# Kernel tuning notes

Measured on AMD Instinct MI355X. Metric: run time of the kernel, lower is better.

The kernel has to match this reference:

```python
import math
import jax, jax.numpy as jnp
import numpy as np

HIDDEN = 768
HEADS = 12
HEAD_DIM = HIDDEN // HEADS  # 64
NUM_BUCKETS = 32            # T5-style relative position bias defaults
MAX_DIST = 128
EPS = 1e-6


def _rel_buckets(T):
    # T5 bidirectional relative-position bucketing, computed statically in numpy.
    ctx = np.arange(T)[:, None]
    mem = np.arange(T)[None, :]
    rp = mem - ctx                     # (T, T)
    nb = NUM_BUCKETS // 2
    ret = (rp > 0).astype(np.int64) * nb
    n = np.abs(rp)
    max_exact = nb // 2
    is_small = n < max_exact
    val_large = max_exact + (
        np.log(np.maximum(n, 1) / max_exact) / math.log(MAX_DIST / max_exact) * (nb - max_exact)
    ).astype(np.int64)
    val_large = np.minimum(val_large, nb - 1)
    ret = ret + np.where(is_small, n, val_large)
    return ret  # (T, T) int


def _layernorm(x, scale, bias):
    mu = jnp.mean(x, axis=-1, keepdims=True)
    var = jnp.mean((x - mu) ** 2, axis=-1, keepdims=True)
    return (x - mu) * jax.lax.rsqrt(var + EPS) * scale + bias


def _rms_groupnorm(x, weight):
    # x: (N, C, H, W, D); RMS over (channels-in-group, spatial), per-channel scale.
    N, C, H, W, D = x.shape
    xg = x.reshape(N, HEADS, C // HEADS, H, W, D)
    ms = jnp.mean(xg * xg, axis=(2, 3, 4, 5), keepdims=True)
    xg = xg * jax.lax.rsqrt(ms + EPS)
    return xg.reshape(N, C, H, W, D) * weight[None, :, None, None, None]


def _forward(x, norm1_weight, input_head_weight, input_head_bias,
             qnorm_scale, qnorm_bias, knorm_scale, knorm_bias,
             rel_bias_table, output_head_weight, output_head_bias):
    T, B, C, H, W, D = x.shape
    residual = x
    xn = _rms_groupnorm(x.reshape(T * B, C, H, W, D), norm1_weight)
    # 1x1 conv QKV as channels-last matmul
    w_in = input_head_weight[:, :, 0, 0, 0]                       # (3C, C)
    xt = jnp.transpose(xn, (0, 2, 3, 4, 1))                        # (TB, H, W, D, C)
    qkv = xt @ w_in.T + input_head_bias                            # (TB, H, W, D, 3C)
    # '(t b) (he c) h w d -> (b h w d) he t c'  with c = 3*head_dim
    qkv = qkv.reshape(T, B, H, W, D, HEADS, 3 * HEAD_DIM)
    qkv = jnp.transpose(qkv, (1, 2, 3, 4, 5, 0, 6))                # (B,H,W,D,He,T,3hd)
    qkv = qkv.reshape(B * H * W * D, HEADS, T, 3 * HEAD_DIM)
    q, k, v = jnp.split(qkv, 3, axis=-1)                           # each (N, He, T, hd)
    q = _layernorm(q, qnorm_scale, qnorm_bias)
    k = _layernorm(k, knorm_scale, knorm_bias)
    # relative position bias (bidirectional)
    buckets = jnp.asarray(_rel_buckets(T))                         # (T, T)
    bias = jnp.transpose(rel_bias_table[buckets], (2, 0, 1))[None]  # (1, He, T, T)
    scale = 1.0 / math.sqrt(HEAD_DIM)
    attn = jax.nn.softmax(jnp.einsum('bhsc,bhtc->bhst', q, k) * scale + bias, axis=-1)
    out = jnp.einsum('bhst,bhtc->bhsc', attn, v)                   # (N, He, T, hd)
    # '(b h w d) he t c -> (t b) (he c) h w d'
    out = out.reshape(B, H, W, D, HEADS, T, HEAD_DIM)
    out = jnp.transpose(out, (5, 0, 4, 6, 1, 2, 3))                # (T,B,He,hd,H,W,D)
    out = out.reshape(T * B, C, H, W, D)
    # output 1x1 conv
    w_out = output_head_weight[:, :, 0, 0, 0]                      # (C, C)
    ot = jnp.transpose(out, (0, 2, 3, 4, 1)) @ w_out.T + output_head_bias
    y = jnp.transpose(ot, (0, 4, 1, 2, 3)).reshape(T, B, C, H, W, D)
    return y + residual


def setup_inputs() -> dict:
    key = jax.random.key(0)
    ks = jax.random.split(key, 4)
    T, B, C, H, W, D = 16, 1, HIDDEN, 16, 16, 8
    x = jax.random.normal(ks[0], (T, B, C, H, W, D), dtype=jnp.float32)
    lecun = 1.0 / math.sqrt(HIDDEN)
    return {
        'x': x,
        'norm1_weight': jnp.ones((HIDDEN,), jnp.float32),
        'input_head_weight': jax.random.normal(ks[1], (3 * HIDDEN, HIDDEN, 1, 1, 1), jnp.float32) * lecun,
        'input_head_bias': jnp.zeros((3 * HIDDEN,), jnp.float32),
        'qnorm_scale': jnp.ones((HEAD_DIM,), jnp.float32),
        'qnorm_bias': jnp.zeros((HEAD_DIM,), jnp.float32),
        'knorm_scale': jnp.ones((HEAD_DIM,), jnp.float32),
        'knorm_bias': jnp.zeros((HEAD_DIM,), jnp.float32),
        'rel_bias_table': jax.random.normal(ks[2], (NUM_BUCKETS, HEADS), jnp.float32) * 0.02,
        'output_head_weight': jax.random.normal(ks[3], (HIDDEN, HIDDEN, 1, 1, 1), jnp.float32) * lecun,
        'output_head_bias': jnp.zeros((HIDDEN,), jnp.float32),
    }


def reference(x, norm1_weight, input_head_weight, input_head_bias,
              qnorm_scale, qnorm_bias, knorm_scale, knorm_bias,
              rel_bias_table, output_head_weight, output_head_bias):
    return _forward(x, norm1_weight, input_head_weight, input_head_bias,
                    qnorm_scale, qnorm_bias, knorm_scale, knorm_bias,
                    rel_bias_table, output_head_weight, output_head_bias)
```

## Files before the change

### kernel.cpp

```cpp
#include <hip/hip_runtime.h>
#include <stdint.h>

#define Tt 16
#define Cc 768
#define Ss 2048
#define N1 2304
#define NH 12
#define HD 64
#define EPSV 1e-6f

typedef unsigned short ushort_t;
typedef __attribute__((ext_vector_type(8))) short short8;
typedef __attribute__((ext_vector_type(4))) short short4v;
typedef __attribute__((ext_vector_type(4))) float f32x4;

static __device__ __forceinline__ float b2f(unsigned short u) {
  union { unsigned int i; float f; } c;
  c.i = ((unsigned int)u) << 16;
  return c.f;
}
static __device__ __forceinline__ unsigned short f2b(float f) {
  union { float f; unsigned int i; } c;
  c.f = f;
  return (unsigned short)((c.i + 0x7fffu + ((c.i >> 16) & 1u)) >> 16);
}

static __device__ __forceinline__ void load8(const void* p, size_t eoff,
                                             int isf32, float* o) {
  if (isf32) {
    const float* f = (const float*)p + eoff;
    f32x4 a = *(const f32x4*)f;
    f32x4 b = *(const f32x4*)(f + 4);
    o[0] = a[0]; o[1] = a[1]; o[2] = a[2]; o[3] = a[3];
    o[4] = b[0]; o[5] = b[1]; o[6] = b[2]; o[7] = b[3];
  } else {
    short8 d = *(const short8*)((const ushort_t*)p + eoff);
#pragma unroll
    for (int e = 0; e < 8; e++) o[e] = b2f((unsigned short)d[e]);
  }
}
static __device__ __forceinline__ float load1(const void* p, size_t eoff, int isf32) {
  return isf32 ? ((const float*)p)[eoff] : b2f(((const ushort_t*)p)[eoff]);
}

#define GLP(p) ((const __attribute__((address_space(1))) void*)(p))
#define LDSP(p) ((__attribute__((address_space(3))) void*)(p))

__global__ __launch_bounds__(256) void detect_k(const ushort_t* __restrict__ x,
                                               int* __restrict__ flag) {
  __shared__ int sbad;
  if (threadIdx.x == 0) sbad = 0;
  __syncthreads();
  int bad = 0;
  for (int i = threadIdx.x; i < 65536; i += 256) {
    const unsigned int e = (x[i] >> 7) & 0xFFu;
    if (e == 0xFFu) bad = 1;
  }
  if (bad) atomicOr(&sbad, 1);
  __syncthreads();
  if (threadIdx.x == 0) flag[0] = sbad;
}

__global__ __launch_bounds__(256) void cvt_big_k(const void* __restrict__ src,
                                                ushort_t* __restrict__ dst,
                                                int n8, const int* __restrict__ flag) {
  const int isf32 = *flag;
  const int i = blockIdx.x * 256 + threadIdx.x;
  if (i >= n8) return;
  float o[8];
  load8(src, (size_t)i * 8, isf32, o);
  short8 v;
#pragma unroll
  for (int e = 0; e < 8; e++) v[e] = (short)f2b(o[e]);
  *(short8*)(dst + (size_t)i * 8) = v;
}

__global__ __launch_bounds__(256) void cvt_small_k(
    const void* w1, const void* bin, const void* bo, const void* qs,
    const void* qb, const void* ks, const void* kb, const void* relb,
    ushort_t* __restrict__ dst, const int* __restrict__ flag) {
  const int isf32 = *flag;
  const void* srcs[8] = {w1, bin, bo, qs, qb, ks, kb, relb};
  const int sizes[8] = {768, 2304, 768, 64, 64, 64, 64, 384};
  int off = 0;
#pragma unroll
  for (int s = 0; s < 8; s++) {
    for (int i = threadIdx.x; i < sizes[s]; i += 256)
      dst[off + i] = isf32 ? f2b(((const float*)srcs[s])[i])
                           : ((const ushort_t*)srcs[s])[i];
    off += sizes[s];
  }
}

__global__ __launch_bounds__(256) void rms_stats_k(
    const void* __restrict__ x, const int* __restrict__ flag,
    float* __restrict__ invrms) {
  const int isf32 = *flag;
  const int t = blockIdx.x / NH;
  const int g = blockIdx.x % NH;
  const size_t base = ((size_t)(t * Cc + g * 64)) * Ss;
  float ss = 0.f;
  for (int v = threadIdx.x; v < 16384; v += 256) {
    const int ci = v >> 8;
    const int sj = (v & 255) << 3;
    float o[8];
    load8(x, base + (size_t)ci * Ss + sj, isf32, o);
#pragma unroll
    for (int e = 0; e < 8; e++) ss += o[e] * o[e];
  }
#pragma unroll
  for (int m = 1; m < 64; m <<= 1) ss += __shfl_xor(ss, m);
  __shared__ float red[4];
  if ((threadIdx.x & 63) == 0) red[threadIdx.x >> 6] = ss;
  __syncthreads();
  if (threadIdx.x == 0) {
    float tot = red[0] + red[1] + red[2] + red[3];
    invrms[blockIdx.x] = rsqrtf(tot * (1.f / 131072.f) + EPSV);
  }
}

__global__ __launch_bounds__(256) void norm_chunk_k(
    const void* __restrict__ x, const int* __restrict__ flag,
    const ushort_t* __restrict__ w1, const float* __restrict__ invrms,
    ushort_t* __restrict__ xnc, int s0c, int chl) {
  __shared__ __align__(16) ushort_t tile[64][64];
  const int isf32 = *flag;
  const int t = blockIdx.z;
  const int c0 = blockIdx.y * 64;
  const int sl0 = blockIdx.x * 64;
  const float ir = invrms[t * NH + (c0 >> 6)];
  const int tid = threadIdx.x;
  for (int v = tid; v < 512; v += 256) {
    const int ci = v >> 3;
    const int q = v & 7;
    float o[8];
    load8(x, ((size_t)(t * Cc + c0 + ci)) * Ss + s0c + sl0 + q * 8, isf32, o);
    const float sc = ir * b2f(w1[c0 + ci]);
    short8 w;
#pragma unroll
    for (int e = 0; e < 8; e++) w[e] = (short)f2b(o[e] * sc);
    *(short8*)&tile[ci][(q ^ (ci >> 3)) * 8] = w;
  }
  __syncthreads();
  for (int v = tid; v < 512; v += 256) {
    const int sj = v >> 3;
    const int cb = (v & 7) * 8;
    const int sw = (sj >> 3) ^ (v & 7);
    const int so = sj & 7;
    short8 o;
#pragma unroll
    for (int e = 0; e < 8; e++) o[e] = (short)tile[cb + e][sw * 8 + so];
    *(short8*)(xnc + ((size_t)(t * chl + sl0 + sj)) * Cc + c0 + cb) = o;
  }
}

__global__ __launch_bounds__(256, 2) void gemm_qkv_k(
    const ushort_t* __restrict__ A, const ushort_t* __restrict__ Bw,
    const ushort_t* __restrict__ bias, ushort_t* __restrict__ Cout) {
  __shared__ __align__(16) ushort_t As[128 * 32];
  __shared__ __align__(16) ushort_t Bs[128 * 32];
  const int tid = threadIdx.x;
  const int bm0 = blockIdx.x * 128;
  const int bn0 = blockIdx.y * 128;
  const int lane = tid & 63;
  const int wave = tid >> 6;
  const int wm = (wave >> 1) << 6;
  const int wn = (wave & 1) << 6;
  f32x4 acc[4][4];
#pragma unroll
  for (int i = 0; i < 4; i++)
#pragma unroll
    for (int j = 0; j < 4; j++) acc[i][j] = (f32x4){0.f, 0.f, 0.f, 0.f};
  const int srow = tid >> 2;
  const int scol = (tid & 3) << 3;
  const ushort_t* ag = A + (size_t)(bm0 + srow) * Cc + scol;
  const ushort_t* bg = Bw + (size_t)(bn0 + srow) * Cc + scol;
  ushort_t* la = As + tid * 8;
  ushort_t* lb = Bs + tid * 8;
  const int frow = lane & 15;
  const int koff = (lane >> 4) << 3;
  for (int kt = 0; kt < Cc; kt += 32) {
    __syncthreads();
    __builtin_amdgcn_global_load_lds(GLP(ag + kt), LDSP(la), 16, 0, 0);
    __builtin_amdgcn_global_load_lds(GLP(ag + kt + 64 * Cc), LDSP(la + 2048), 16, 0, 0);
    __builtin_amdgcn_global_load_lds(GLP(bg + kt), LDSP(lb), 16, 0, 0);
    __builtin_amdgcn_global_load_lds(GLP(bg + kt + 64 * Cc), LDSP(lb + 2048), 16, 0, 0);
    __syncthreads();
    short8 af[4], bf[4];
#pragma unroll
    for (int i = 0; i < 4; i++)
      af[i] = *(const short8*)(As + (wm + i * 16 + frow) * 32 + koff);
#pragma unroll
    for (int j = 0; j < 4; j++)
      bf[j] = *(const short8*)(Bs + (wn + j * 16 + frow) * 32 + koff);
#pragma unroll
    for (int i = 0; i < 4; i++)
#pragma unroll
      for (int j = 0; j < 4; j++)
        acc[i][j] = __builtin_amdgcn_mfma_f32_16x16x32_bf16(af[i], bf[j], acc[i][j], 0, 0, 0);
  }
  const int mq = (lane >> 4) << 2;
  const int nl = lane & 15;
#pragma unroll
  for (int j = 0; j < 4; j++) {
    const int col = bn0 + wn + j * 16 + nl;
    const float bc = b2f(bias[col]);
#pragma unroll
    for (int i = 0; i < 4; i++) {
#pragma unroll
      for (int r = 0; r < 4; r++) {
        const int row = bm0 + wm + i * 16 + mq + r;
        Cout[(size_t)row * N1 + col] = f2b(acc[i][j][r] + bc);
      }
    }
  }
}

__global__ __launch_bounds__(256) void attention_k(
    const ushort_t* __restrict__ qkvc, const ushort_t* __restrict__ qs,
    const ushort_t* __restrict__ qb, const ushort_t* __restrict__ ks,
    const ushort_t* __restrict__ kb, const ushort_t* __restrict__ relb,
    ushort_t* __restrict__ aoc, int chl) {
  __shared__ __align__(16) float qf[4][16][68];
  __shared__ __align__(16) float kf[4][16][68];
  __shared__ __align__(16) float vf[4][16][68];
  __shared__ __align__(16) float attw[4][16][20];
  __shared__ __align__(16) float lnw[4][64];
  const int tid = threadIdx.x;
  const int wave = tid >> 6;
  const int lane = tid & 63;
  if (tid < 64) {
    lnw[0][tid] = b2f(qs[tid]);
    lnw[1][tid] = b2f(qb[tid]);
    lnw[2][tid] = b2f(ks[tid]);
    lnw[3][tid] = b2f(kb[tid]);
  }
  const int p = blockIdx.x * 4 + wave;
  const int sl = p / 12;
  const int h = p - sl * 12;
  const ushort_t* src = qkvc + (size_t)sl * N1 + h * 192;
  const size_t tstride = (size_t)chl * N1;
#pragma unroll
  for (int t = 0; t < 16; t++) {
    const ushort_t* r = src + (size_t)t * tstride;
    qf[wave][t][lane] = b2f(r[lane]);
    kf[wave][t][lane] = b2f(r[64 + lane]);
    vf[wave][t][lane] = b2f(r[128 + lane]);
  }
  __syncthreads();
  {
    const int row = lane >> 1;
    const int half = lane & 1;
    float* buf = (row < 16) ? &qf[wave][row][0] : &kf[wave][row - 16][0];
    const float* sc = (row < 16) ? lnw[0] : lnw[2];
    const float* bi = (row < 16) ? lnw[1] : lnw[3];
    f32x4* bp = (f32x4*)(buf + half * 32);
    f32x4 v4[8];
    float s = 0.f;
#pragma unroll
    for (int q4 = 0; q4 < 8; q4++) {
      v4[q4] = bp[q4];
      s += v4[q4][0] + v4[q4][1] + v4[q4][2] + v4[q4][3];
    }
    s += __shfl_xor(s, 1);
    const float mu = s * (1.f / 64.f);
    float va = 0.f;
#pragma unroll
    for (int q4 = 0; q4 < 8; q4++) {
#pragma unroll
      for (int e = 0; e < 4; e++) {
        const float d = v4[q4][e] - mu;
        va += d * d;
      }
    }
    va += __shfl_xor(va, 1);
    const float rs = rsqrtf(va * (1.f / 64.f) + EPSV);
    const f32x4* sc4 = (const f32x4*)(sc + half * 32);
    const f32x4* bi4 = (const f32x4*)(bi + half * 32);
#pragma unroll
    for (int q4 = 0; q4 < 8; q4++) {
      f32x4 scv = sc4[q4], biv = bi4[q4], o;
#pragma unroll
      for (int e = 0; e < 4; e++) o[e] = (v4[q4][e] - mu) * rs * scv[e] + biv[e];
      bp[q4] = o;
    }
  }
  __syncthreads();
  const int g = lane >> 4;
  const int t2 = lane & 15;
#pragma unroll
  for (int it = 0; it < 4; it++) {
    const int t1 = it * 4 + g;
    const f32x4* qrow = (const f32x4*)&qf[wave][t1][0];
    const f32x4* krow = (const f32x4*)&kf[wave][t2][0];
    float sco = 0.f;
#pragma unroll
    for (int q4 = 0; q4 < 16; q4++) {
      f32x4 a = qrow[q4], b = krow[q4];
      sco += a[0] * b[0] + a[1] * b[1] + a[2] * b[2] + a[3] * b[3];
    }
    const int rp = t2 - t1;
    int bkt = (rp > 0) ? 16 : 0;
    const int n = (rp < 0) ? -rp : rp;
    if (n < 8) {
      bkt += n;
    } else {
      int vl = 8 + (int)(__logf((float)n * 0.125f) * 2.8853900817779268f);
      bkt += (vl < 15) ? vl : 15;
    }
    sco = sco * 0.125f + b2f(relb[bkt * NH + h]);
    float mx = sco;
#pragma unroll
    for (int m = 8; m >= 1; m >>= 1) mx = fmaxf(mx, __shfl_xor(mx, m));
    const float ex = __expf(sco - mx);
    float sm = ex;
#pragma unroll
    for (int m = 8; m >= 1; m >>= 1) sm += __shfl_xor(sm, m);
    attw[wave][t1][t2] = ex / sm;
  }
  __syncthreads();
  const int jq = lane & 15;
#pragma unroll
  for (int it = 0; it < 4; it++) {
    const int t1 = it * 4 + g;
    const f32x4* arow = (const f32x4*)&attw[wave][t1][0];
    f32x4 o = (f32x4){0.f, 0.f, 0.f, 0.f};
#pragma unroll
    for (int tq = 0; tq < 4; tq++) {
      f32x4 aw = arow[tq];
#pragma unroll
      for (int e = 0; e < 4; e++) {
        f32x4 vv = *(const f32x4*)&vf[wave][tq * 4 + e][jq * 4];
        o[0] += aw[e] * vv[0];
        o[1] += aw[e] * vv[1];
        o[2] += aw[e] * vv[2];
        o[3] += aw[e] * vv[3];
      }
    }
    short4v st;
#pragma unroll
    for (int e = 0; e < 4; e++) st[e] = (short)f2b(o[e]);
    *(short4v*)(aoc + ((size_t)(t1 * chl + sl)) * Cc + h * HD + jq * 4) = st;
  }
}

__global__ __launch_bounds__(256, 2) void gemm_out_k(
    const ushort_t* __restrict__ A, const ushort_t* __restrict__ Bm,
    const ushort_t* __restrict__ bias, const void* __restrict__ xres,
    const int* __restrict__ flag, float* __restrict__ y, int s0c,
    int chl, int lgchl) {
  __shared__ __align__(16) ushort_t As[128 * 32];
  __shared__ __align__(16) ushort_t Bs[128 * 32];
  const int isf32 = *flag;
  const int tid = threadIdx.x;
  const int bm0 = blockIdx.x * 128;
  const int bn0 = blockIdx.y * 128;
  const int lane = tid & 63;
  const int wave = tid >> 6;
  const int wm = (wave >> 1) << 6;
  const int wn = (wave & 1) << 6;
  f32x4 acc[4][4];
#pragma unroll
  for (int i = 0; i < 4; i++)
#pragma unroll
    for (int j = 0; j < 4; j++) acc[i][j] = (f32x4){0.f, 0.f, 0.f, 0.f};
  const int srow = tid >> 2;
  const int scol = (tid & 3) << 3;
  const ushort_t* ag = A + (size_t)(bm0 + srow) * Cc + scol;
  const ushort_t* bg = Bm + (size_t)(bn0 + srow) * Cc + scol;
  ushort_t* la = As + tid * 8;
  ushort_t* lb = Bs + tid * 8;
  const int frow = lane & 15;
  const int koff = (lane >> 4) << 3;
  for (int kt = 0; kt < Cc; kt += 32) {
    __syncthreads();
    __builtin_amdgcn_global_load_lds(GLP(ag + kt), LDSP(la), 16, 0, 0);
    __builtin_amdgcn_global_load_lds(GLP(ag + kt + 64 * Cc), LDSP(la + 2048), 16, 0, 0);
    __builtin_amdgcn_global_load_lds(GLP(bg + kt), LDSP(lb), 16, 0, 0);
    __builtin_amdgcn_global_load_lds(GLP(bg + kt + 64 * Cc), LDSP(lb + 2048), 16, 0, 0);
    __syncthreads();
    short8 af[4], bf[4];
#pragma unroll
    for (int i = 0; i < 4; i++)
      af[i] = *(const short8*)(As + (wm + i * 16 + frow) * 32 + koff);
#pragma unroll
    for (int j = 0; j < 4; j++)
      bf[j] = *(const short8*)(Bs + (wn + j * 16 + frow) * 32 + koff);
#pragma unroll
    for (int i = 0; i < 4; i++)
#pragma unroll
      for (int j = 0; j < 4; j++)
        acc[i][j] = __builtin_amdgcn_mfma_f32_16x16x32_bf16(af[i], bf[j], acc[i][j], 0, 0, 0);
  }
  const int mq = (lane >> 4) << 2;
  const int nl = lane & 15;
#pragma unroll
  for (int j = 0; j < 4; j++) {
    const int col = bn0 + wn + j * 16 + nl;
    const int t = col >> lgchl;
    const int sp = s0c + (col & (chl - 1));
#pragma unroll
    for (int i = 0; i < 4; i++) {
#pragma unroll
      for (int r = 0; r < 4; r++) {
        const int cch = bm0 + wm + i * 16 + mq + r;
        const size_t off = ((size_t)(t * Cc + cch)) * Ss + sp;
        y[off] = acc[i][j][r] + b2f(bias[cch]) + load1(xres, off, isf32);
      }
    }
  }
}

extern "C" void kernel_launch(void* const* d_in, const int* in_sizes, int n_in,
                              void* d_out, int out_size, void* d_ws, size_t ws_size,
                              hipStream_t stream) {
  (void)in_sizes; (void)n_in; (void)out_size;
  const void* x   = d_in[0];
  const void* w1  = d_in[1];
  const void* win = d_in[2];
  const void* bin = d_in[3];
  const void* qsc = d_in[4];
  const void* qbi = d_in[5];
  const void* ksc = d_in[6];
  const void* kbi = d_in[7];
  const void* rbt = d_in[8];
  const void* wo  = d_in[9];
  const void* bo  = d_in[10];
  float* y = (float*)d_out;

  char* ws = (char*)d_ws;
  int* flag      = (int*)ws;
  float* invrms  = (float*)(ws + 1024);
  ushort_t* smallw = (ushort_t*)(ws + 4096);
  ushort_t* w1b  = smallw;
  ushort_t* binb = smallw + 768;
  ushort_t* bob  = smallw + 3072;
  ushort_t* qsb  = smallw + 3840;
  ushort_t* qbb  = smallw + 3904;
  ushort_t* ksb  = smallw + 3968;
  ushort_t* kbb  = smallw + 4032;
  ushort_t* relbb = smallw + 4096;
  ushort_t* winb = (ushort_t*)(ws + 20480);
  ushort_t* wob  = (ushort_t*)(ws + 3559424);
  const size_t fixed = 4739072;

  const size_t per_row = (size_t)(Cc * 2 + N1 * 2 + Cc * 2);
  int chl = Ss;
  while (chl > 64 && fixed + (size_t)Tt * chl * per_row > ws_size) chl >>= 1;
  int lgchl = 0;
  while ((1 << (lgchl + 1)) <= chl) lgchl++;

  ushort_t* xnc  = (ushort_t*)(ws + fixed);
  ushort_t* qkvc = xnc + (size_t)Tt * chl * Cc;
  ushort_t* aoc  = qkvc + (size_t)Tt * chl * N1;

  detect_k<<<1, 256, 0, stream>>>((const ushort_t*)x, flag);
  cvt_small_k<<<1, 256, 0, stream>>>(w1, bin, bo, qsc, qbi, ksc, kbi, rbt, smallw, flag);
  cvt_big_k<<<1769472 / 8 / 256, 256, 0, stream>>>(win, winb, 1769472 / 8, flag);
  cvt_big_k<<<589824 / 8 / 256, 256, 0, stream>>>(wo, wob, 589824 / 8, flag);
  rms_stats_k<<<dim3(Tt * NH), 256, 0, stream>>>(x, flag, invrms);
  for (int s0c = 0; s0c < Ss; s0c += chl) {
    norm_chunk_k<<<dim3(chl / 64, Cc / 64, Tt), 256, 0, stream>>>(x, flag, w1b, invrms, xnc, s0c, chl);
    gemm_qkv_k<<<dim3(Tt * chl / 128, N1 / 128), 256, 0, stream>>>(xnc, winb, binb, qkvc);
    attention_k<<<dim3(chl * NH / 4), 256, 0, stream>>>(qkvc, qsb, qbb, ksb, kbb, relbb, aoc, chl);
    gemm_out_k<<<dim3(Cc / 128, Tt * chl / 128), 256, 0, stream>>>(wob, aoc, bob, x, flag, y, s0c, chl, lgchl);
  }
}
```

Before: 712.7 us.

## Add 256x256-tile QKV GEMM with LDS double buffering and block swizzle

```diff
diff --git a/kernel.cpp b/kernel.cpp
--- a/kernel.cpp
+++ b/kernel.cpp
@@ -216,6 +216,119 @@
   }
 }
 
+static __device__ __forceinline__ void rdA_q(short8 af[4][2], const ushort_t* base,
+                                             int arow, int half, const int ckk[2]) {
+#pragma unroll
+  for (int mi = 0; mi < 4; mi++)
+#pragma unroll
+    for (int kk = 0; kk < 2; kk++)
+      af[mi][kk] = *(const short8*)&base[arow + half * 4096 + mi * 1024 + ckk[kk]];
+}
+static __device__ __forceinline__ void rdB_q(short8 bf[2][2], const ushort_t* base,
+                                             int brow, int nib, const int ckk[2]) {
+#pragma unroll
+  for (int ni = 0; ni < 2; ni++)
+#pragma unroll
+    for (int kk = 0; kk < 2; kk++)
+      bf[ni][kk] = *(const short8*)&base[brow + (nib + ni) * 1024 + ckk[kk]];
+}
+template <int MIB, int NIB>
+static __device__ __forceinline__ void mm8_q(f32x4 (&acc)[8][4], const short8 af[4][2],
+                                             const short8 bf[2][2]) {
+#pragma unroll
+  for (int mi = 0; mi < 4; mi++)
+#pragma unroll
+    for (int ni = 0; ni < 2; ni++)
+#pragma unroll
+      for (int kk = 0; kk < 2; kk++)
+        acc[MIB + mi][NIB + ni] = __builtin_amdgcn_mfma_f32_16x16x32_bf16(
+            af[mi][kk], bf[ni][kk], acc[MIB + mi][NIB + ni], 0, 0, 0);
+}
+
+__global__ __launch_bounds__(512, 2) void gemm_qkv256_k(
+    const ushort_t* __restrict__ A, const ushort_t* __restrict__ Bw,
+    const ushort_t* __restrict__ bias, ushort_t* __restrict__ Cout) {
+  __shared__ __align__(16) ushort_t lds[2][2][16384];
+  const int tid = threadIdx.x;
+  const int lane = tid & 63;
+  const int wave = tid >> 6;
+  const int wr = wave >> 2;
+  const int wc = wave & 3;
+  const int wg = ((int)blockIdx.x & 7) * 144 + ((int)blockIdx.x >> 3);
+  const int bm0 = (wg / 9) * 256;
+  const int bn0 = (wg % 9) * 256;
+  const int srow = tid >> 3;
+  const int scol = ((tid & 7) ^ (srow & 7)) << 3;
+  const ushort_t* ag = A + (size_t)(bm0 + srow) * Cc + scol;
+  const ushort_t* bg = Bw + (size_t)(bn0 + srow) * Cc + scol;
+#define QSTG(p, kt) { \
+    __builtin_amdgcn_global_load_lds(GLP(ag + (kt)), LDSP(&lds[p][0][tid * 8]), 16, 0, 0); \
+    __builtin_amdgcn_global_load_lds(GLP(ag + 64 * Cc + (kt)), LDSP(&lds[p][0][4096 + tid * 8]), 16, 0, 0); \
+    __builtin_amdgcn_global_load_lds(GLP(ag + 128 * Cc + (kt)), LDSP(&lds[p][0][8192 + tid * 8]), 16, 0, 0); \
+    __builtin_amdgcn_global_load_lds(GLP(ag + 192 * Cc + (kt)), LDSP(&lds[p][0][12288 + tid * 8]), 16, 0, 0); \
+    __builtin_amdgcn_global_load_lds(GLP(bg + (kt)), LDSP(&lds[p][1][tid * 8]), 16, 0, 0); \
+    __builtin_amdgcn_global_load_lds(GLP(bg + 64 * Cc + (kt)), LDSP(&lds[p][1][4096 + tid * 8]), 16, 0, 0); \
+    __builtin_amdgcn_global_load_lds(GLP(bg + 128 * Cc + (kt)), LDSP(&lds[p][1][8192 + tid * 8]), 16, 0, 0); \
+    __builtin_amdgcn_global_load_lds(GLP(bg + 192 * Cc + (kt)), LDSP(&lds[p][1][12288 + tid * 8]), 16, 0, 0); \
+  }
+  const int koffb = (lane >> 4) << 4;
+  const int lsw = (lane & 7) << 4;
+  const int ckk[2] = {(koffb ^ lsw) >> 1, ((64 + koffb) ^ lsw) >> 1};
+  const int arow = (wr * 128 + (lane & 15)) * 64;
+  const int brow = (wc * 64 + (lane & 15)) * 64;
+  f32x4 acc[8][4];
+#pragma unroll
+  for (int i = 0; i < 8; i++)
+#pragma unroll
+    for (int j = 0; j < 4; j++) acc[i][j] = (f32x4){0.f, 0.f, 0.f, 0.f};
+  QSTG(0, 0);
+  __syncthreads();
+  for (int i = 0; i < 12; i++) {
+    const int p = i & 1;
+    if (i < 11) QSTG(p ^ 1, (i + 1) * 64);
+    __builtin_amdgcn_sched_barrier(0);
+    const ushort_t* Ab = &lds[p][0][0];
+    const ushort_t* Bb = &lds[p][1][0];
+    short8 af[4][2], bf0[2][2], bf1[2][2];
+    rdA_q(af, Ab, arow, 0, ckk);
+    rdB_q(bf0, Bb, brow, 0, ckk);
+    __builtin_amdgcn_s_setprio(1);
+    mm8_q<0, 0>(acc, af, bf0);
+    __builtin_amdgcn_s_setprio(0);
+    __builtin_amdgcn_sched_barrier(0);
+    rdB_q(bf1, Bb, brow, 2, ckk);
+    __builtin_amdgcn_s_setprio(1);
+    mm8_q<0, 2>(acc, af, bf1);
+    __builtin_amdgcn_s_setprio(0);
+    __builtin_amdgcn_sched_barrier(0);
+    rdA_q(af, Ab, arow, 1, ckk);
+    __builtin_amdgcn_s_setprio(1);
+    mm8_q<4, 0>(acc, af, bf0);
+    __builtin_amdgcn_s_setprio(0);
+    __builtin_amdgcn_sched_barrier(0);
+    __builtin_amdgcn_s_setprio(1);
+    mm8_q<4, 2>(acc, af, bf1);
+    __builtin_amdgcn_s_setprio(0);
+    if (i < 11) __syncthreads();
+  }
+  const int mq = (lane >> 4) << 2;
+  const int nl = lane & 15;
+#pragma unroll
+  for (int ni = 0; ni < 4; ni++) {
+    const int col = bn0 + wc * 64 + ni * 16 + nl;
+    const float bc = b2f(bias[col]);
+#pragma unroll
+    for (int mi = 0; mi < 8; mi++) {
+#pragma unroll
+      for (int r = 0; r < 4; r++) {
+        const int row = bm0 + wr * 128 + mi * 16 + mq + r;
+        Cout[(size_t)row * N1 + col] = f2b(acc[mi][ni][r] + bc);
+      }
+    }
+  }
+#undef QSTG
+}
+
 __global__ __launch_bounds__(256) void attention_k(
     const ushort_t* __restrict__ qkvc, const ushort_t* __restrict__ qs,
     const ushort_t* __restrict__ qb, const ushort_t* __restrict__ ks,
@@ -323,11 +436,11 @@
 #pragma unroll
   for (int it = 0; it < 4; it++) {
     const int t1 = it * 4 + g;
-    const f32x4* arow = (const f32x4*)&attw[wave][t1][0];
+    const f32x4* arow2 = (const f32x4*)&attw[wave][t1][0];
     f32x4 o = (f32x4){0.f, 0.f, 0.f, 0.f};
 #pragma unroll
     for (int tq = 0; tq < 4; tq++) {
-      f32x4 aw = arow[tq];
+      f32x4 aw = arow2[tq];
 #pragma unroll
       for (int e = 0; e < 4; e++) {
         f32x4 vv = *(const f32x4*)&vf[wave][tq * 4 + e][jq * 4];
@@ -353,8 +466,19 @@
   __shared__ __align__(16) ushort_t Bs[128 * 32];
   const int isf32 = *flag;
   const int tid = threadIdx.x;
-  const int bm0 = blockIdx.x * 128;
-  const int bn0 = blockIdx.y * 128;
+  int bmt = blockIdx.x, bnt = blockIdx.y;
+  {
+    const int nwg = gridDim.x * gridDim.y;
+    if ((nwg & 7) == 0) {
+      const int hw = (int)blockIdx.x + (int)blockIdx.y * gridDim.x;
+      const int cpx = nwg >> 3;
+      const int w = (hw & 7) * cpx + (hw >> 3);
+      bmt = w % gridDim.x;
+      bnt = w / gridDim.x;
+    }
+  }
+  const int bm0 = bmt * 128;
+  const int bn0 = bnt * 128;
   const int lane = tid & 63;
   const int wave = tid >> 6;
   const int wm = (wave >> 1) << 6;
@@ -430,7 +554,6 @@
 
   char* ws = (char*)d_ws;
   int* flag      = (int*)ws;
-  float* invrms  = (float*)(ws + 1024);
   ushort_t* smallw = (ushort_t*)(ws + 4096);
   ushort_t* w1b  = smallw;
   ushort_t* binb = smallw + 768;
@@ -440,6 +563,7 @@
   ushort_t* ksb  = smallw + 3968;
   ushort_t* kbb  = smallw + 4032;
   ushort_t* relbb = smallw + 4096;
+  float* invrms  = (float*)(ws + 1024);
   ushort_t* winb = (ushort_t*)(ws + 20480);
   ushort_t* wob  = (ushort_t*)(ws + 3559424);
   const size_t fixed = 4739072;
@@ -461,7 +585,11 @@
   rms_stats_k<<<dim3(Tt * NH), 256, 0, stream>>>(x, flag, invrms);
   for (int s0c = 0; s0c < Ss; s0c += chl) {
     norm_chunk_k<<<dim3(chl / 64, Cc / 64, Tt), 256, 0, stream>>>(x, flag, w1b, invrms, xnc, s0c, chl);
-    gemm_qkv_k<<<dim3(Tt * chl / 128, N1 / 128), 256, 0, stream>>>(xnc, winb, binb, qkvc);
+    if (chl == Ss) {
+      gemm_qkv256_k<<<dim3(1152), 512, 0, stream>>>(xnc, winb, binb, qkvc);
+    } else {
+      gemm_qkv_k<<<dim3(Tt * chl / 128, N1 / 128), 256, 0, stream>>>(xnc, winb, binb, qkvc);
+    }
     attention_k<<<dim3(chl * NH / 4), 256, 0, stream>>>(qkvc, qsb, qbb, ksb, kbb, relbb, aoc, chl);
     gemm_out_k<<<dim3(Cc / 128, Tt * chl / 128), 256, 0, stream>>>(wob, aoc, bob, x, flag, y, s0c, chl, lgchl);
   }
```

Result: faster. 685.6 us (-3.8%).
